# Performance work log

Measured on AMD Instinct MI355X. Metric: run time of the kernel, lower is better.

The kernel has to match this reference:

```python
import jax, jax.numpy as jnp
import numpy as np

T_MAX = 26  # hardcoded 26 char steps in the torch module

def _resize(x, hw):
    # torch F.interpolate bilinear, align_corners=False (half-pixel) == jax linear, no antialias
    return jax.image.resize(x, x.shape[:-2] + hw, method='linear', antialias=False)

def _ce(logits, labels):
    # per-element cross entropy, labels int
    logp = jax.nn.log_softmax(logits, axis=-1)
    return -jnp.take_along_axis(logp, labels[:, None].astype(jnp.int32), axis=-1)[:, 0]


def setup_inputs() -> dict:
    key = jax.random.key(0)
    ks = jax.random.split(key, 6)
    b, H, W, L = 512, 32, 128, 64
    hm, wm, hl, wl = 16, 64, 8, 32
    return {
        'masks': jax.random.uniform(ks[0], (b, 1, H, W), dtype=jnp.float32),
        'backfore_feature': jax.random.normal(ks[1], (b, 2, H, W), dtype=jnp.float32),
        'seq1_attention_map': jax.random.uniform(ks[2], (b, L, T_MAX), dtype=jnp.float32),
        'char_middle': jax.random.normal(ks[3], (b, 27, hm, wm), dtype=jnp.float32),
        'char_low': jax.random.normal(ks[4], (b, 27, hl, wl), dtype=jnp.float32),
        'length': jax.random.randint(ks[5], (b,), 2, 27),
        'iteration': 1000,
        'alpha': jnp.float32(0.1),
    }


def reference(masks, backfore_feature, seq1_attention_map, char_middle, char_low, length, iteration, alpha):
    b, _, H, W = masks.shape
    f32 = masks.dtype
    masks_i = (masks > 0.5).astype(jnp.int32)                      # [b,1,H,W]
    sm = jax.nn.softmax(backfore_feature, axis=1)                  # [b,2,H,W]

    # ---- SegLoss: CE applied to softmax probs as if logits (faithful to torch) ----
    per_elem = _ce(sm.transpose(0, 2, 3, 1).reshape(-1, 2), masks_i.reshape(-1))
    if iteration > 20000:
        value = per_elem.reshape(b, -1).mean(1)
        sel = (value < 1.0).astype(f32)
        predmask_loss = (value * sel).sum() / jnp.maximum(sel.sum(), 1.0)
    else:
        predmask_loss = per_elem.mean()

    fore_mask = (sm[:, 1] > 0.5).astype(jnp.int32)[:, None]        # [b,1,H,W], int -> no grad
    Attn = jnp.transpose(seq1_attention_map, (0, 2, 1))            # [b,26,L]
    n = length - 1                                                  # valid chars per sample
    nf = n.astype(f32)
    row_valid = (jnp.arange(T_MAX)[None, :] < n[:, None]).astype(f32)  # [b,26]

    # ---- Correct_1D_Location (seg mask detached; Attn gets grads) ----
    fore_d = jax.lax.stop_gradient(fore_mask)
    interp = _resize(Attn[:, None], (T_MAX, W))[:, 0]              # [b,26,W]
    # pairwise sum_{i<j} sum_w (v_i v_j)^2 over the first n rows, vectorized
    sq = jnp.square(interp) * row_valid[:, :, None]
    S = sq.sum(1)
    S2 = jnp.square(sq).sum(1)
    irrelevant = (0.5 * (jnp.square(S) - S2).sum(-1) / nf).sum()
    act = jax.nn.sigmoid(70.0 * (interp - 0.1)) * row_valid[:, :, None]
    # sum_t act[t,w] * mask[h,w] == (sum_t act)[w] * mask[h,w]
    char_sum = jnp.clip(act.sum(1)[:, None, :] * fore_d[:, 0].astype(f32), 0.0, 1.0)  # [b,H,W]
    single2 = jnp.stack([1.0 - char_sum, char_sum], axis=-1)       # [b,H,W,2]
    correct_loss = _ce(single2.reshape(-1, 2), fore_d.reshape(-1)).mean() + irrelevant

    # ---- Char_Segmention_Loss (attention and fore mask detached) ----
    attn_clr = jax.lax.stop_gradient(Attn) * row_valid[:, :, None]  # clear_noise

    def char_branch(char_feat):
        h, w = char_feat.shape[2], char_feat.shape[3]
        fm = (_resize(fore_d.astype(f32), (h, w)) >= 0.4).astype(jnp.int32)   # [b,1,h,w]
        ai = _resize(attn_clr[:, None], (T_MAX, w))[:, 0]
        ab = (ai > alpha).astype(jnp.int32)                                   # [b,26,w]
        single = ab[:, :, None, :] * fm                                       # [b,26,h,w]
        mask27 = jnp.concatenate([1 - fm, single], axis=1)                    # [b,27,h,w]
        labels = jnp.argmax(mask27, axis=1).reshape(-1)
        cel = _ce(char_feat.transpose(0, 2, 3, 1).reshape(-1, 27), labels).mean()
        soft = jax.nn.softmax(char_feat, axis=1)
        m1 = soft[:, 1:].reshape(b, T_MAX, -1)
        m2 = mask27[:, 1:].astype(f32).reshape(b, T_MAX, -1)
        inter = (m1 * m2).sum(-1)
        score = (2.0 * inter + 1.0) / (m1.sum(-1) + m2.sum(-1) + 1.0)         # [b,26]
        dice = (((1.0 - score) * row_valid).sum(-1) / nf).sum() / b
        return cel + dice, mask27, soft

    loss_middle, _, soft_mid = char_branch(char_middle)
    loss_low, mask_low, soft_low = char_branch(char_low)

    return (predmask_loss, correct_loss, loss_low, loss_middle,
            mask_low, soft_mid[:, 1:], soft_low[:, 1:])
```

## Files before the change

### kernel.cpp

```cpp
#include <hip/hip_runtime.h>
#include <math.h>

#define NB 512
#define TT 26
#define LL 64
#define HH 32
#define WW 128

typedef unsigned long long ull;

__device__ __forceinline__ float wave_sum(float v) {
#pragma unroll
  for (int o = 32; o > 0; o >>= 1) v += __shfl_xor(v, o, 64);
  return v;
}

template<int CTRL, int RM>
__device__ __forceinline__ float dpp_add(float x) {
  int y = __builtin_amdgcn_update_dpp(0, __float_as_int(x), CTRL, RM, 0xf, true);
  return x + __int_as_float(y);
}
__device__ __forceinline__ float wave_red63(float x) {
  x = dpp_add<0x111, 0xf>(x);
  x = dpp_add<0x112, 0xf>(x);
  x = dpp_add<0x114, 0xf>(x);
  x = dpp_add<0x118, 0xf>(x);
  x = dpp_add<0x142, 0xa>(x);
  x = dpp_add<0x143, 0xc>(x);
  return x;
}

__global__ __launch_bounds__(1024) void k_mega(
    const float* __restrict__ masks, const float* __restrict__ bf,
    const float* __restrict__ seq, const float* __restrict__ cm,
    const float* __restrict__ cl, const int* __restrict__ length,
    const float* __restrict__ alpha_p,
    float* __restrict__ out_mask, float* __restrict__ out_smid,
    float* __restrict__ out_slow,
    float* __restrict__ seg_part, float* __restrict__ cor_part,
    float* __restrict__ irr_part, float* __restrict__ celm_part,
    float* __restrict__ cell_part,
    float* __restrict__ inter_mid, float* __restrict__ m1s_mid, float* __restrict__ m2s_mid,
    float* __restrict__ inter_low, float* __restrict__ m1s_low, float* __restrict__ m2s_low)
{
  int b = blockIdx.x;
  int tid = threadIdx.x;
  int lane = tid & 63, wv = tid >> 6;

  __shared__ float att[LL * TT];
  __shared__ float wsA_lds[WW];
  __shared__ ull s_bits[TT];
  __shared__ unsigned s_alow[TT];
  __shared__ unsigned s_cols_mid[64];
  __shared__ unsigned s_cols_low[32];
  __shared__ ull fmsk_lds[64];
  __shared__ ull s_fmrow[16];
  __shared__ unsigned fmrow32[8];
  __shared__ float s_red_in[16][TT], s_red_m1[16][TT];
  __shared__ float s_ce[16];
  __shared__ float ps[16], pc[16];
  __shared__ float wpart[2];

  int n = length[b] - 1;
  float alpha = alpha_p[0];

  const float* sb = seq + (size_t)b * (LL * TT);
  for (int i = tid; i < LL * TT; i += 1024) att[i] = sb[i];
  __syncthreads();

  if (tid < 128) {
    int w = tid;
    int k = w >> 1;
    int i0, i1; float c0, c1;
    if ((w & 1) == 0) {
      if (k == 0) { i0 = 0; i1 = 0; c0 = 1.f; c1 = 0.f; }
      else        { i0 = k - 1; i1 = k; c0 = 0.25f; c1 = 0.75f; }
    } else {
      if (k == 63) { i0 = 63; i1 = 63; c0 = 1.f; c1 = 0.f; }
      else         { i0 = k; i1 = k + 1; c0 = 0.75f; c1 = 0.25f; }
    }
    float S = 0.f, S2 = 0.f, A = 0.f;
    for (int t = 0; t < n; ++t) {
      float v = c0 * att[i0 * TT + t] + c1 * att[i1 * TT + t];
      float s = v * v;
      S += s; S2 += s * s;
      A += 1.f / (1.f + __expf(-70.f * (v - 0.1f)));
    }
    wsA_lds[w] = A;
    float c = S * S - S2;
    c = wave_sum(c);
    if (lane == 0) wpart[wv] = c;
  }
  if (tid < 64) {
    int x = tid;
    for (int t = 0; t < TT; ++t) {
      bool pred = (t < n) && (att[x * TT + t] > alpha);
      ull m = __ballot(pred);
      if (x == 0) s_bits[t] = m;
    }
  } else if (tid < 128) {
    int x = tid - 64;
    for (int t = 0; t < TT; ++t) {
      bool pred = (x < 32) && (t < n) &&
                  (0.5f * (att[(2 * x) * TT + t] + att[(2 * x + 1) * TT + t]) > alpha);
      ull m = __ballot(pred);
      if (x == 0) s_alow[t] = (unsigned)m;
    }
  }
  __syncthreads();
  if (tid == 0) irr_part[b] = 0.5f * (wpart[0] + wpart[1]) / (float)n;

  if (tid < 64) {
    unsigned cb = 0;
#pragma unroll
    for (int t = 0; t < TT; ++t) cb |= (unsigned)((s_bits[t] >> tid) & 1ULL) << t;
    s_cols_mid[tid] = cb;
  } else if (tid < 96) {
    int xc = tid - 64;
    unsigned cb = 0;
#pragma unroll
    for (int t = 0; t < TT; ++t) cb |= ((s_alow[t] >> xc) & 1u) << t;
    s_cols_low[xc] = cb;
  }

  {
    const float* mb = masks + (size_t)b * 4096;
    const float* fb = bf + (size_t)b * 8192;
    float A = wsA_lds[tid & 127];
    float cs = fminf(fmaxf(A, 0.f), 1.f);
    float ce_fore = log1pf(__expf(1.f - 2.f * cs));
    float seg_acc = 0.f, cor_acc = 0.f;
    for (int k = 0; k < 4; ++k) {
      int px = k * 1024 + tid;
      float m = mb[px];
      float b0 = fb[px];
      float b1 = fb[4096 + px];
      float mx = fmaxf(b0, b1);
      float e0 = __expf(b0 - mx), e1 = __expf(b1 - mx);
      float inv = 1.f / (e0 + e1);
      float p0 = e0 * inv, p1 = e1 * inv;
      float pm = fmaxf(p0, p1);
      float lse = pm + log1pf(__expf(-fabsf(p1 - p0)));
      seg_acc += lse - ((m > 0.5f) ? p1 : p0);
      bool fore = b1 > b0;
      cor_acc += fore ? ce_fore : 0.313261687518222834f;
      ull fbm = __ballot(fore);
      if (lane == 0) fmsk_lds[k * 16 + wv] = fbm;
    }
    seg_acc = wave_red63(seg_acc);
    cor_acc = wave_red63(cor_acc);
    if (lane == 63) { ps[wv] = seg_acc; pc[wv] = cor_acc; }
  }
  __syncthreads();
  if (tid == 0) {
    float s = 0.f, c = 0.f;
#pragma unroll
    for (int i = 0; i < 16; ++i) { s += ps[i]; c += pc[i]; }
    seg_part[b] = s;
    cor_part[b] = c;
  }

  {
    int y = wv;
    int x = tid & 63;
    int word = x >> 5;
    int p = (x & 31) * 2;
    ull r0 = fmsk_lds[4 * y + word];
    ull r1 = fmsk_lds[4 * y + 2 + word];
    int cnt = (int)((r0 >> p) & 1) + (int)((r0 >> (p + 1)) & 1)
            + (int)((r1 >> p) & 1) + (int)((r1 >> (p + 1)) & 1);
    bool fm = cnt >= 2;
    unsigned cbk = s_cols_mid[x];
    int lab = (fm && cbk) ? __ffs((int)cbk) : 0;
    if (!fm) cbk = 0;
    ull bmv = __ballot(fm);
    if (lane == 0) s_fmrow[wv] = bmv;

    const float* base = cm + (size_t)b * 27 * 1024 + tid;
    float v[27];
    float xl = 0.f, s0 = 0.f;
#pragma unroll
    for (int c = 0; c < 27; ++c) {
      float r = base[(size_t)c * 1024];
      xl = (c == lab) ? r : xl;
      r = __expf(r);
      v[c] = r;
      s0 += r;
    }
    float inv0 = 1.f / s0;
    float ce_part = __logf(s0) - xl;

    float* os = out_smid + (size_t)b * 26 * 1024 + tid;
#pragma unroll
    for (int t = 0; t < TT; ++t) {
      float m1 = v[t + 1] * inv0;
      os[(size_t)t * 1024] = m1;
      float ri = wave_red63(((cbk >> t) & 1) ? m1 : 0.f);
      float rm = wave_red63(m1);
      if (lane == 63) { s_red_in[wv][t] = ri; s_red_m1[wv][t] = rm; }
    }
    float rce = wave_red63(ce_part);
    if (lane == 63) s_ce[wv] = rce;
  }
  __syncthreads();
  if (tid < TT) {
    float m2v = 0.f;
#pragma unroll
    for (int r = 0; r < 16; ++r) m2v += (float)__popcll(s_fmrow[r] & s_bits[tid]);
    float si = 0.f, sm = 0.f;
#pragma unroll
    for (int w = 0; w < 16; ++w) { si += s_red_in[w][tid]; sm += s_red_m1[w][tid]; }
    int o = b * TT + tid;
    m2s_mid[o] = m2v;
    inter_mid[o] = si;
    m1s_mid[o] = sm;
  }
  if (tid == TT) {
    float c16 = 0.f;
#pragma unroll
    for (int w = 0; w < 16; ++w) c16 += s_ce[w];
    celm_part[b] = c16;
  }
  __syncthreads();

  if (tid < 256) {
    int px = tid;
    int y = px >> 5, x = px & 31;
    int wb = 4 * x + 1;
    int word = wb >> 6;
    int p = wb & 63;
    ull r0 = fmsk_lds[(4 * y + 1) * 2 + word];
    ull r1 = fmsk_lds[(4 * y + 2) * 2 + word];
    int cnt = (int)((r0 >> p) & 1) + (int)((r0 >> (p + 1)) & 1)
            + (int)((r1 >> p) & 1) + (int)((r1 >> (p + 1)) & 1);
    bool fm = cnt >= 2;
    unsigned cbk = s_cols_low[x];
    int lab = (fm && cbk) ? __ffs((int)cbk) : 0;
    if (!fm) cbk = 0;
    ull bmv = __ballot(fm);
    if (lane == 0) {
      fmrow32[2 * wv] = (unsigned)bmv;
      fmrow32[2 * wv + 1] = (unsigned)(bmv >> 32);
    }

    const float* base = cl + (size_t)b * 27 * 256 + px;
    float v[27];
    float xl = 0.f, s0 = 0.f;
#pragma unroll
    for (int c = 0; c < 27; ++c) {
      float r = base[(size_t)c * 256];
      xl = (c == lab) ? r : xl;
      r = __expf(r);
      v[c] = r;
      s0 += r;
    }
    float inv0 = 1.f / s0;
    float ce_part = __logf(s0) - xl;

    float* om  = out_mask + (size_t)b * 27 * 256 + px;
    float* osf = out_slow + (size_t)b * 26 * 256 + px;
    om[0] = fm ? 0.f : 1.f;
#pragma unroll
    for (int t = 0; t < TT; ++t) {
      float m1 = v[t + 1] * inv0;
      osf[(size_t)t * 256] = m1;
      bool m2 = (cbk >> t) & 1;
      om[(size_t)(t + 1) * 256] = m2 ? 1.f : 0.f;
      float ri = wave_red63(m2 ? m1 : 0.f);
      float rm = wave_red63(m1);
      if (lane == 63) { s_red_in[wv][t] = ri; s_red_m1[wv][t] = rm; }
    }
    float rce = wave_red63(ce_part);
    if (lane == 63) s_ce[wv] = rce;
  }
  __syncthreads();
  if (tid < TT) {
    float m2v = 0.f;
#pragma unroll
    for (int yy = 0; yy < 8; ++yy) m2v += (float)__popc(fmrow32[yy] & s_alow[tid]);
    float si = 0.f, sm = 0.f;
#pragma unroll
    for (int w = 0; w < 4; ++w) { si += s_red_in[w][tid]; sm += s_red_m1[w][tid]; }
    int o = b * TT + tid;
    m2s_low[o] = m2v;
    inter_low[o] = si;
    m1s_low[o] = sm;
  }
  if (tid == TT) cell_part[b] = s_ce[0] + s_ce[1] + s_ce[2] + s_ce[3];
}

__global__ __launch_bounds__(1024) void k_final(
    const float* __restrict__ seg_part, const float* __restrict__ cor_part,
    const float* __restrict__ irr_part, const float* __restrict__ celm_part,
    const float* __restrict__ cell_part,
    const float* __restrict__ inter_mid, const float* __restrict__ m1s_mid,
    const float* __restrict__ m2s_mid,
    const float* __restrict__ inter_low, const float* __restrict__ m1s_low,
    const float* __restrict__ m2s_low,
    const int* __restrict__ length, const int* __restrict__ iter_p,
    float* __restrict__ out)
{
  int tid = threadIdx.x;
  float dm = 0.f, dl = 0.f;
  for (int i = tid; i < NB * TT; i += 1024) {
    int b = i / TT, t = i - b * TT;
    int n = length[b] - 1;
    if (t < n) {
      float inv_n = 1.f / (float)n;
      dm += (1.f - (2.f * inter_mid[i] + 1.f) / (m1s_mid[i] + m2s_mid[i] + 1.f)) * inv_n;
      dl += (1.f - (2.f * inter_low[i] + 1.f) / (m1s_low[i] + m2s_low[i] + 1.f)) * inv_n;
    }
  }
  float ss = 0.f, sel = 0.f, ssel = 0.f;
  float irr = 0.f, cell = 0.f, celm = 0.f, cor = 0.f;
  for (int b = tid; b < NB; b += 1024) {
    float v = seg_part[b];
    ss += v;
    float val = v * (1.f / 4096.f);
    if (val < 1.f) { sel += 1.f; ssel += val; }
    irr += irr_part[b]; cell += cell_part[b]; celm += celm_part[b]; cor += cor_part[b];
  }

  dm = wave_sum(dm); dl = wave_sum(dl); ss = wave_sum(ss);
  sel = wave_sum(sel); ssel = wave_sum(ssel);
  irr = wave_sum(irr); celm = wave_sum(celm); cell = wave_sum(cell);
  cor = wave_sum(cor);
  __shared__ float red[9][16];
  int wv = tid >> 6;
  if ((tid & 63) == 0) {
    red[0][wv] = dm; red[1][wv] = dl; red[2][wv] = ss; red[3][wv] = sel;
    red[4][wv] = ssel; red[5][wv] = irr; red[6][wv] = celm; red[7][wv] = cell;
    red[8][wv] = cor;
  }
  __syncthreads();
  if (tid == 0) {
    float a[9];
#pragma unroll
    for (int j = 0; j < 9; ++j) {
      float s = 0.f;
      for (int i = 0; i < 16; ++i) s += red[j][i];
      a[j] = s;
    }
    float pred = (iter_p[0] > 20000) ? (a[4] / fmaxf(a[3], 1.f)) : (a[2] / 2097152.f);
    out[0] = pred;
    out[1] = a[8] / 2097152.f + a[5];
    out[2] = a[7] / 131072.f + a[1] / 512.f;
    out[3] = a[6] / 524288.f + a[0] / 512.f;
  }
}

extern "C" void kernel_launch(void* const* d_in, const int* in_sizes, int n_in,
                              void* d_out, int out_size, void* d_ws, size_t ws_size,
                              hipStream_t stream) {
  (void)in_sizes; (void)n_in; (void)out_size; (void)ws_size;
  const float* masks  = (const float*)d_in[0];
  const float* bf     = (const float*)d_in[1];
  const float* seq    = (const float*)d_in[2];
  const float* cmid   = (const float*)d_in[3];
  const float* clow   = (const float*)d_in[4];
  const int*   length = (const int*)d_in[5];
  const int*   iter   = (const int*)d_in[6];
  const float* alpha  = (const float*)d_in[7];
  float* out = (float*)d_out;

  char* ws = (char*)d_ws;
  float* seg_part  = (float*)(ws + 0);
  float* cor_part  = (float*)(ws + 2048);
  float* irr_part  = (float*)(ws + 4096);
  float* celm_part = (float*)(ws + 6144);
  float* cell_part = (float*)(ws + 8192);
  float* inter_mid = (float*)(ws + 10240);
  float* m1s_mid   = (float*)(ws + 63488);
  float* m2s_mid   = (float*)(ws + 116736);
  float* inter_low = (float*)(ws + 169984);
  float* m1s_low   = (float*)(ws + 223232);
  float* m2s_low   = (float*)(ws + 276480);

  float* out_mask = out + 4;
  float* out_smid = out + 4 + 3538944;
  float* out_slow = out + 4 + 3538944 + 13631488;

  k_mega<<<NB, 1024, 0, stream>>>(masks, bf, seq, cmid, clow, length, alpha,
                                  out_mask, out_smid, out_slow,
                                  seg_part, cor_part, irr_part, celm_part, cell_part,
                                  inter_mid, m1s_mid, m2s_mid,
                                  inter_low, m1s_low, m2s_low);
  k_final<<<1, 1024, 0, stream>>>(seg_part, cor_part, irr_part, celm_part, cell_part,
                                  inter_mid, m1s_mid, m2s_mid,
                                  inter_low, m1s_low, m2s_low, length, iter, out);
}
```

Baseline: 65.63 us.

## Split mega kernel into pre-pass and LDS-staged char kernel with vectorized I/O

The single per-sample mega kernel is split into a small 256-thread pre-pass, which computes the seg/correct losses and the attention and foreground bitmasks into workspace, and a character kernel. The character kernel stages the char logits and softmax outputs through LDS so global loads and stores use float4, and it replaces per-t wave reductions with per-wave column sums. The low-resolution branch gets its own blocks, each handling four samples, so it runs in parallel with the mid branch. The cost is an extra kernel launch, a workspace round trip for the bitmasks, and about 62KB of LDS per block, which limits occupancy.

```diff
diff --git a/kernel.cpp b/kernel.cpp
--- a/kernel.cpp
+++ b/kernel.cpp
@@ -3,11 +3,9 @@
 
 #define NB 512
 #define TT 26
-#define LL 64
-#define HH 32
-#define WW 128
 
 typedef unsigned long long ull;
+typedef unsigned int u32;
 
 __device__ __forceinline__ float wave_sum(float v) {
 #pragma unroll
@@ -30,47 +28,27 @@
   return x;
 }
 
-__global__ __launch_bounds__(1024) void k_mega(
+__global__ __launch_bounds__(256) void k_pre(
     const float* __restrict__ masks, const float* __restrict__ bf,
-    const float* __restrict__ seq, const float* __restrict__ cm,
-    const float* __restrict__ cl, const int* __restrict__ length,
+    const float* __restrict__ seq, const int* __restrict__ length,
     const float* __restrict__ alpha_p,
-    float* __restrict__ out_mask, float* __restrict__ out_smid,
-    float* __restrict__ out_slow,
+    ull* __restrict__ amid, u32* __restrict__ alow, ull* __restrict__ fmsk,
     float* __restrict__ seg_part, float* __restrict__ cor_part,
-    float* __restrict__ irr_part, float* __restrict__ celm_part,
-    float* __restrict__ cell_part,
-    float* __restrict__ inter_mid, float* __restrict__ m1s_mid, float* __restrict__ m2s_mid,
-    float* __restrict__ inter_low, float* __restrict__ m1s_low, float* __restrict__ m2s_low)
+    float* __restrict__ irr_part)
 {
-  int b = blockIdx.x;
-  int tid = threadIdx.x;
-  int lane = tid & 63, wv = tid >> 6;
-
-  __shared__ float att[LL * TT];
-  __shared__ float wsA_lds[WW];
-  __shared__ ull s_bits[TT];
-  __shared__ unsigned s_alow[TT];
-  __shared__ unsigned s_cols_mid[64];
-  __shared__ unsigned s_cols_low[32];
-  __shared__ ull fmsk_lds[64];
-  __shared__ ull s_fmrow[16];
-  __shared__ unsigned fmrow32[8];
-  __shared__ float s_red_in[16][TT], s_red_m1[16][TT];
-  __shared__ float s_ce[16];
-  __shared__ float ps[16], pc[16];
-  __shared__ float wpart[2];
-
+  int b = blockIdx.x, tid = threadIdx.x, lane = tid & 63, wv = tid >> 6;
+  __shared__ float att[64 * TT];
+  __shared__ float wsA[128];
+  __shared__ float wpart[2], ps[4], pc[4];
+  const float4* sb4 = (const float4*)(seq + (size_t)b * (64 * TT));
+  float4* att4 = (float4*)att;
+  for (int i = tid; i < 416; i += 256) att4[i] = sb4[i];
+  __syncthreads();
   int n = length[b] - 1;
   float alpha = alpha_p[0];
 
-  const float* sb = seq + (size_t)b * (LL * TT);
-  for (int i = tid; i < LL * TT; i += 1024) att[i] = sb[i];
-  __syncthreads();
-
   if (tid < 128) {
-    int w = tid;
-    int k = w >> 1;
+    int w = tid, k = w >> 1;
     int i0, i1; float c0, c1;
     if ((w & 1) == 0) {
       if (k == 0) { i0 = 0; i1 = 0; c0 = 1.f; c1 = 0.f; }
@@ -86,7 +64,7 @@
       S += s; S2 += s * s;
       A += 1.f / (1.f + __expf(-70.f * (v - 0.1f)));
     }
-    wsA_lds[w] = A;
+    wsA[w] = A;
     float c = S * S - S2;
     c = wave_sum(c);
     if (lane == 0) wpart[wv] = c;
@@ -96,7 +74,7 @@
     for (int t = 0; t < TT; ++t) {
       bool pred = (t < n) && (att[x * TT + t] > alpha);
       ull m = __ballot(pred);
-      if (x == 0) s_bits[t] = m;
+      if (x == 0) amid[(size_t)b * TT + t] = m;
     }
   } else if (tid < 128) {
     int x = tid - 64;
@@ -104,189 +82,287 @@
       bool pred = (x < 32) && (t < n) &&
                   (0.5f * (att[(2 * x) * TT + t] + att[(2 * x + 1) * TT + t]) > alpha);
       ull m = __ballot(pred);
-      if (x == 0) s_alow[t] = (unsigned)m;
+      if (x == 0) alow[(size_t)b * TT + t] = (u32)m;
     }
   }
   __syncthreads();
   if (tid == 0) irr_part[b] = 0.5f * (wpart[0] + wpart[1]) / (float)n;
 
-  if (tid < 64) {
-    unsigned cb = 0;
-#pragma unroll
-    for (int t = 0; t < TT; ++t) cb |= (unsigned)((s_bits[t] >> tid) & 1ULL) << t;
-    s_cols_mid[tid] = cb;
-  } else if (tid < 96) {
-    int xc = tid - 64;
-    unsigned cb = 0;
-#pragma unroll
-    for (int t = 0; t < TT; ++t) cb |= ((s_alow[t] >> xc) & 1u) << t;
-    s_cols_low[xc] = cb;
-  }
-
-  {
-    const float* mb = masks + (size_t)b * 4096;
-    const float* fb = bf + (size_t)b * 8192;
-    float A = wsA_lds[tid & 127];
-    float cs = fminf(fmaxf(A, 0.f), 1.f);
-    float ce_fore = log1pf(__expf(1.f - 2.f * cs));
-    float seg_acc = 0.f, cor_acc = 0.f;
-    for (int k = 0; k < 4; ++k) {
-      int px = k * 1024 + tid;
-      float m = mb[px];
-      float b0 = fb[px];
-      float b1 = fb[4096 + px];
-      float mx = fmaxf(b0, b1);
-      float e0 = __expf(b0 - mx), e1 = __expf(b1 - mx);
-      float inv = 1.f / (e0 + e1);
-      float p0 = e0 * inv, p1 = e1 * inv;
-      float pm = fmaxf(p0, p1);
-      float lse = pm + log1pf(__expf(-fabsf(p1 - p0)));
-      seg_acc += lse - ((m > 0.5f) ? p1 : p0);
-      bool fore = b1 > b0;
-      cor_acc += fore ? ce_fore : 0.313261687518222834f;
-      ull fbm = __ballot(fore);
-      if (lane == 0) fmsk_lds[k * 16 + wv] = fbm;
-    }
-    seg_acc = wave_red63(seg_acc);
-    cor_acc = wave_red63(cor_acc);
-    if (lane == 63) { ps[wv] = seg_acc; pc[wv] = cor_acc; }
-  }
+  const float* mb = masks + (size_t)b * 4096;
+  const float* fb = bf + (size_t)b * 8192;
+  float A = wsA[tid & 127];
+  float cs = fminf(fmaxf(A, 0.f), 1.f);
+  float ce_fore = log1pf(__expf(1.f - 2.f * cs));
+  float seg_acc = 0.f, cor_acc = 0.f;
+  for (int k = 0; k < 16; ++k) {
+    int px = k * 256 + tid;
+    float m = mb[px];
+    float b0 = fb[px];
+    float b1 = fb[4096 + px];
+    float mx = fmaxf(b0, b1);
+    float e0 = __expf(b0 - mx), e1 = __expf(b1 - mx);
+    float inv = 1.f / (e0 + e1);
+    float p0 = e0 * inv, p1 = e1 * inv;
+    float pm = fmaxf(p0, p1);
+    float lse = pm + log1pf(__expf(-fabsf(p1 - p0)));
+    seg_acc += lse - ((m > 0.5f) ? p1 : p0);
+    bool fore = b1 > b0;
+    cor_acc += fore ? ce_fore : 0.313261687518222834f;
+    ull fbm = __ballot(fore);
+    if (lane == 0) fmsk[(size_t)b * 64 + k * 4 + wv] = fbm;
+  }
+  seg_acc = wave_red63(seg_acc);
+  cor_acc = wave_red63(cor_acc);
+  if (lane == 63) { ps[wv] = seg_acc; pc[wv] = cor_acc; }
   __syncthreads();
   if (tid == 0) {
-    float s = 0.f, c = 0.f;
-#pragma unroll
-    for (int i = 0; i < 16; ++i) { s += ps[i]; c += pc[i]; }
-    seg_part[b] = s;
-    cor_part[b] = c;
-  }
-
-  {
-    int y = wv;
-    int x = tid & 63;
-    int word = x >> 5;
-    int p = (x & 31) * 2;
-    ull r0 = fmsk_lds[4 * y + word];
-    ull r1 = fmsk_lds[4 * y + 2 + word];
+    seg_part[b] = ps[0] + ps[1] + ps[2] + ps[3];
+    cor_part[b] = pc[0] + pc[1] + pc[2] + pc[3];
+  }
+}
+
+__global__ __launch_bounds__(1024) void k_chars(
+    const float* __restrict__ cm, const float* __restrict__ cl,
+    const ull* __restrict__ fmsk, const ull* __restrict__ amid,
+    const u32* __restrict__ alow,
+    float* __restrict__ out_mask, float* __restrict__ out_smid,
+    float* __restrict__ out_slow,
+    float* __restrict__ celm_part, float* __restrict__ cell_part,
+    float* __restrict__ inter_mid, float* __restrict__ m1s_mid, float* __restrict__ m2s_mid,
+    float* __restrict__ inter_low, float* __restrict__ m1s_low, float* __restrict__ m2s_low)
+{
+  int blk = blockIdx.x, tid = threadIdx.x, lane = tid & 63, wv = tid >> 6;
+  __shared__ __align__(16) char smem[62816];
+
+  if (blk < NB) {
+    float*  bufF   = (float*)smem;
+    float4* buf4   = (float4*)smem;
+    u32*    cbkA   = (u32*)(smem + 57344);
+    ull*    s_bits = (ull*)(smem + 61440);
+    ull*    s_fmw  = (ull*)(smem + 61648);
+    u32*    s_cols = (u32*)(smem + 62160);
+    ull*    s_fmrow= (ull*)(smem + 62416);
+    float*  red_in = (float*)(smem + 62544);
+    float*  red_m1 = (float*)(smem + 62648);
+    float*  s_ce   = (float*)(smem + 62752);
+    int b = blk, px = tid, x = lane, y = wv;
+
+    if (tid < TT) s_bits[tid] = amid[(size_t)b * TT + tid];
+    else if (tid >= 32 && tid < 96) s_fmw[tid - 32] = fmsk[(size_t)b * 64 + (tid - 32)];
+    const float4* cm4 = (const float4*)(cm + (size_t)b * 27648);
+    for (int i = tid; i < 3584; i += 1024) buf4[i] = cm4[i];
+    __syncthreads();
+    if (tid < 64) {
+      u32 cb = 0;
+#pragma unroll
+      for (int t = 0; t < TT; ++t) cb |= (u32)((s_bits[t] >> tid) & 1ULL) << t;
+      s_cols[tid] = cb;
+    }
+    float v[27];
+#pragma unroll
+    for (int c = 0; c < 14; ++c) v[c] = bufF[c * 1024 + px];
+    __syncthreads();
+    for (int i = tid; i < 3328; i += 1024) buf4[i] = cm4[3584 + i];
+    __syncthreads();
+#pragma unroll
+    for (int c = 14; c < 27; ++c) v[c] = bufF[(c - 14) * 1024 + px];
+
+    int word = x >> 5, p = (x & 31) * 2;
+    ull r0 = s_fmw[4 * y + word], r1 = s_fmw[4 * y + 2 + word];
     int cnt = (int)((r0 >> p) & 1) + (int)((r0 >> (p + 1)) & 1)
             + (int)((r1 >> p) & 1) + (int)((r1 >> (p + 1)) & 1);
     bool fm = cnt >= 2;
-    unsigned cbk = s_cols_mid[x];
+    u32 cbk = s_cols[x];
     int lab = (fm && cbk) ? __ffs((int)cbk) : 0;
     if (!fm) cbk = 0;
     ull bmv = __ballot(fm);
     if (lane == 0) s_fmrow[wv] = bmv;
-
-    const float* base = cm + (size_t)b * 27 * 1024 + tid;
-    float v[27];
+    cbkA[px] = cbk;
+
     float xl = 0.f, s0 = 0.f;
 #pragma unroll
     for (int c = 0; c < 27; ++c) {
-      float r = base[(size_t)c * 1024];
+      float r = v[c];
       xl = (c == lab) ? r : xl;
-      r = __expf(r);
-      v[c] = r;
-      s0 += r;
+      float e = __expf(r);
+      v[c] = e;
+      s0 += e;
     }
     float inv0 = 1.f / s0;
-    float ce_part = __logf(s0) - xl;
-
-    float* os = out_smid + (size_t)b * 26 * 1024 + tid;
-#pragma unroll
-    for (int t = 0; t < TT; ++t) {
-      float m1 = v[t + 1] * inv0;
-      os[(size_t)t * 1024] = m1;
-      float ri = wave_red63(((cbk >> t) & 1) ? m1 : 0.f);
-      float rm = wave_red63(m1);
-      if (lane == 63) { s_red_in[wv][t] = ri; s_red_m1[wv][t] = rm; }
-    }
-    float rce = wave_red63(ce_part);
+    float rce = wave_red63(__logf(s0) - xl);
     if (lane == 63) s_ce[wv] = rce;
-  }
-  __syncthreads();
-  if (tid < TT) {
-    float m2v = 0.f;
-#pragma unroll
-    for (int r = 0; r < 16; ++r) m2v += (float)__popcll(s_fmrow[r] & s_bits[tid]);
-    float si = 0.f, sm = 0.f;
-#pragma unroll
-    for (int w = 0; w < 16; ++w) { si += s_red_in[w][tid]; sm += s_red_m1[w][tid]; }
-    int o = b * TT + tid;
-    m2s_mid[o] = m2v;
-    inter_mid[o] = si;
-    m1s_mid[o] = sm;
-  }
-  if (tid == TT) {
-    float c16 = 0.f;
-#pragma unroll
-    for (int w = 0; w < 16; ++w) c16 += s_ce[w];
-    celm_part[b] = c16;
-  }
-  __syncthreads();
-
-  if (tid < 256) {
-    int px = tid;
-    int y = px >> 5, x = px & 31;
-    int wb = 4 * x + 1;
-    int word = wb >> 6;
-    int p = wb & 63;
-    ull r0 = fmsk_lds[(4 * y + 1) * 2 + word];
-    ull r1 = fmsk_lds[(4 * y + 2) * 2 + word];
-    int cnt = (int)((r0 >> p) & 1) + (int)((r0 >> (p + 1)) & 1)
-            + (int)((r1 >> p) & 1) + (int)((r1 >> (p + 1)) & 1);
-    bool fm = cnt >= 2;
-    unsigned cbk = s_cols_low[x];
-    int lab = (fm && cbk) ? __ffs((int)cbk) : 0;
-    if (!fm) cbk = 0;
-    ull bmv = __ballot(fm);
-    if (lane == 0) {
-      fmrow32[2 * wv] = (unsigned)bmv;
-      fmrow32[2 * wv + 1] = (unsigned)(bmv >> 32);
-    }
-
-    const float* base = cl + (size_t)b * 27 * 256 + px;
-    float v[27];
-    float xl = 0.f, s0 = 0.f;
-#pragma unroll
-    for (int c = 0; c < 27; ++c) {
-      float r = base[(size_t)c * 256];
-      xl = (c == lab) ? r : xl;
-      r = __expf(r);
-      v[c] = r;
-      s0 += r;
-    }
-    float inv0 = 1.f / s0;
-    float ce_part = __logf(s0) - xl;
-
-    float* om  = out_mask + (size_t)b * 27 * 256 + px;
-    float* osf = out_slow + (size_t)b * 26 * 256 + px;
-    om[0] = fm ? 0.f : 1.f;
-#pragma unroll
-    for (int t = 0; t < TT; ++t) {
-      float m1 = v[t + 1] * inv0;
-      osf[(size_t)t * 256] = m1;
-      bool m2 = (cbk >> t) & 1;
-      om[(size_t)(t + 1) * 256] = m2 ? 1.f : 0.f;
-      float ri = wave_red63(m2 ? m1 : 0.f);
-      float rm = wave_red63(m1);
-      if (lane == 63) { s_red_in[wv][t] = ri; s_red_m1[wv][t] = rm; }
-    }
-    float rce = wave_red63(ce_part);
-    if (lane == 63) s_ce[wv] = rce;
-  }
-  __syncthreads();
-  if (tid < TT) {
-    float m2v = 0.f;
-#pragma unroll
-    for (int yy = 0; yy < 8; ++yy) m2v += (float)__popc(fmrow32[yy] & s_alow[tid]);
-    float si = 0.f, sm = 0.f;
-#pragma unroll
-    for (int w = 0; w < 4; ++w) { si += s_red_in[w][tid]; sm += s_red_m1[w][tid]; }
-    int o = b * TT + tid;
-    m2s_low[o] = m2v;
-    inter_low[o] = si;
-    m1s_low[o] = sm;
-  }
-  if (tid == TT) cell_part[b] = s_ce[0] + s_ce[1] + s_ce[2] + s_ce[3];
+
+#pragma unroll
+    for (int t = 13; t < 26; ++t) bufF[(t - 13) * 1024 + px] = v[t + 1] * inv0;
+    __syncthreads();
+    float4* smid4 = (float4*)(out_smid + (size_t)b * 26624);
+    for (int i = tid; i < 3328; i += 1024) smid4[3328 + i] = buf4[i];
+    if (wv < 13) {
+      int t = 13 + wv;
+      float isum = 0.f, msum = 0.f;
+#pragma unroll
+      for (int k = 0; k < 16; ++k) {
+        int q = lane + 64 * k;
+        float m1 = bufF[wv * 1024 + q];
+        u32 cb = cbkA[q];
+        msum += m1;
+        isum += ((cb >> t) & 1) ? m1 : 0.f;
+      }
+      isum = wave_red63(isum); msum = wave_red63(msum);
+      if (lane == 63) { red_in[t] = isum; red_m1[t] = msum; }
+    }
+    __syncthreads();
+#pragma unroll
+    for (int t = 0; t < 13; ++t) bufF[t * 1024 + px] = v[t + 1] * inv0;
+    __syncthreads();
+    for (int i = tid; i < 3328; i += 1024) smid4[i] = buf4[i];
+    if (wv < 13) {
+      int t = wv;
+      float isum = 0.f, msum = 0.f;
+#pragma unroll
+      for (int k = 0; k < 16; ++k) {
+        int q = lane + 64 * k;
+        float m1 = bufF[wv * 1024 + q];
+        u32 cb = cbkA[q];
+        msum += m1;
+        isum += ((cb >> t) & 1) ? m1 : 0.f;
+      }
+      isum = wave_red63(isum); msum = wave_red63(msum);
+      if (lane == 63) { red_in[t] = isum; red_m1[t] = msum; }
+    }
+    __syncthreads();
+    if (tid < TT) {
+      float m2v = 0.f;
+#pragma unroll
+      for (int r = 0; r < 16; ++r) m2v += (float)__popcll(s_fmrow[r] & s_bits[tid]);
+      int o = b * TT + tid;
+      m2s_mid[o] = m2v;
+      inter_mid[o] = red_in[tid];
+      m1s_mid[o] = red_m1[tid];
+    }
+    if (tid == TT) {
+      float c16 = 0.f;
+#pragma unroll
+      for (int w = 0; w < 16; ++w) c16 += s_ce[w];
+      celm_part[b] = c16;
+    }
+  } else {
+    int L = blk - NB;
+    float*  bufF    = (float*)smem;
+    float4* buf4    = (float4*)smem;
+    u32*    cbkL    = (u32*)(smem + 55296);
+    u32*    l_bits  = (u32*)(smem + 57344);
+    u32*    colsL   = (u32*)(smem + 57760);
+    ull*    fmw4    = (ull*)(smem + 58272);
+    u32*    fmrow32 = (u32*)(smem + 60320);
+    float*  ceL     = (float*)(smem + 60384);
+
+    if (tid < 104) l_bits[tid] = alow[(size_t)(L * 4) * TT + tid];
+    else if (tid >= 128 && tid < 384) fmw4[tid - 128] = fmsk[(size_t)(L * 4) * 64 + (tid - 128)];
+    __syncthreads();
+    if (tid < 128) {
+      int s = tid >> 5, xx = tid & 31;
+      u32 cb = 0;
+#pragma unroll
+      for (int t = 0; t < TT; ++t) cb |= ((l_bits[s * TT + t] >> xx) & 1u) << t;
+      colsL[tid] = cb;
+    }
+    const float4* cl4 = (const float4*)cl;
+    float4* slow4 = (float4*)out_slow;
+    float4* mask4 = (float4*)out_mask;
+
+    for (int pr = 0; pr < 2; ++pr) {
+      for (int i = tid; i < 3456; i += 1024) {
+        int s = i / 1728, r = i - s * 1728;
+        buf4[i] = cl4[(size_t)(L * 4 + 2 * pr + s) * 1728 + r];
+      }
+      __syncthreads();
+      if (tid < 512) {
+        int s = tid >> 8, sl = 2 * pr + s;
+        int px = tid & 255, y = px >> 5, xx = px & 31;
+        int wb = 4 * xx + 1, word = wb >> 6, pp = wb & 63;
+        ull r0 = fmw4[sl * 64 + (4 * y + 1) * 2 + word];
+        ull r1 = fmw4[sl * 64 + (4 * y + 2) * 2 + word];
+        int cnt = (int)((r0 >> pp) & 1) + (int)((r0 >> (pp + 1)) & 1)
+                + (int)((r1 >> pp) & 1) + (int)((r1 >> (pp + 1)) & 1);
+        bool fm = cnt >= 2;
+        u32 cbk = colsL[sl * 32 + xx];
+        int lab = (fm && cbk) ? __ffs((int)cbk) : 0;
+        if (!fm) cbk = 0;
+        ull bmv = __ballot(fm);
+        if (lane == 0) {
+          fmrow32[s * 8 + 2 * (wv & 3)] = (u32)bmv;
+          fmrow32[s * 8 + 2 * (wv & 3) + 1] = (u32)(bmv >> 32);
+        }
+        float v[27];
+#pragma unroll
+        for (int c = 0; c < 27; ++c) v[c] = bufF[s * 6912 + c * 256 + px];
+        float xl = 0.f, s0 = 0.f;
+#pragma unroll
+        for (int c = 0; c < 27; ++c) {
+          float r = v[c];
+          xl = (c == lab) ? r : xl;
+          float e = __expf(r);
+          v[c] = e;
+          s0 += e;
+        }
+        float inv0 = 1.f / s0;
+        float rce = wave_red63(__logf(s0) - xl);
+        if (lane == 63) ceL[wv] = rce;
+        bufF[s * 6912 + px] = fm ? 0.f : 1.f;
+#pragma unroll
+        for (int t = 0; t < TT; ++t) bufF[s * 6912 + (t + 1) * 256 + px] = v[t + 1] * inv0;
+        cbkL[s * 256 + px] = cbk;
+      }
+      __syncthreads();
+      for (int i = tid; i < 3328; i += 1024) {
+        int s = i / 1664, r = i - s * 1664;
+        slow4[(size_t)(L * 4 + 2 * pr + s) * 1664 + r] = buf4[s * 1728 + 64 + r];
+      }
+      for (int i = tid; i < 3456; i += 1024) {
+        int s = i / 1728, r = i - s * 1728;
+        int c = r >> 6, off = r & 63;
+        float4 o;
+        if (c == 0) o = buf4[s * 1728 + off];
+        else {
+          int t = c - 1;
+          o.x = ((cbkL[s * 256 + off * 4 + 0] >> t) & 1) ? 1.f : 0.f;
+          o.y = ((cbkL[s * 256 + off * 4 + 1] >> t) & 1) ? 1.f : 0.f;
+          o.z = ((cbkL[s * 256 + off * 4 + 2] >> t) & 1) ? 1.f : 0.f;
+          o.w = ((cbkL[s * 256 + off * 4 + 3] >> t) & 1) ? 1.f : 0.f;
+        }
+        mask4[(size_t)(L * 4 + 2 * pr + s) * 1728 + r] = o;
+      }
+      if (tid < 512) {
+        int s = wv >> 2;
+        int bb2 = L * 4 + 2 * pr + s;
+        for (int t = wv & 3; t < TT; t += 4) {
+          float isum = 0.f, msum = 0.f;
+#pragma unroll
+          for (int k = 0; k < 4; ++k) {
+            int q = lane + 64 * k;
+            float m1 = bufF[s * 6912 + (t + 1) * 256 + q];
+            u32 cb = cbkL[s * 256 + q];
+            msum += m1;
+            isum += ((cb >> t) & 1) ? m1 : 0.f;
+          }
+          isum = wave_red63(isum); msum = wave_red63(msum);
+          if (lane == 63) { inter_low[bb2 * TT + t] = isum; m1s_low[bb2 * TT + t] = msum; }
+        }
+      }
+      if (tid >= 512 && tid < 564) {
+        int j = tid - 512;
+        int s = j / TT, t = j - s * TT, sl = 2 * pr + s;
+        float m2v = 0.f;
+#pragma unroll
+        for (int yy = 0; yy < 8; ++yy) m2v += (float)__popc(fmrow32[s * 8 + yy] & l_bits[sl * TT + t]);
+        m2s_low[(L * 4 + sl) * TT + t] = m2v;
+      }
+      if (tid == 600) cell_part[L * 4 + 2 * pr] = ceL[0] + ceL[1] + ceL[2] + ceL[3];
+      if (tid == 601) cell_part[L * 4 + 2 * pr + 1] = ceL[4] + ceL[5] + ceL[6] + ceL[7];
+      __syncthreads();
+    }
+  }
 }
 
 __global__ __launch_bounds__(1024) void k_final(
@@ -320,7 +396,6 @@
     if (val < 1.f) { sel += 1.f; ssel += val; }
     irr += irr_part[b]; cell += cell_part[b]; celm += celm_part[b]; cor += cor_part[b];
   }
-
   dm = wave_sum(dm); dl = wave_sum(dl); ss = wave_sum(ss);
   sel = wave_sum(sel); ssel = wave_sum(ssel);
   irr = wave_sum(irr); celm = wave_sum(celm); cell = wave_sum(cell);
@@ -375,16 +450,21 @@
   float* inter_low = (float*)(ws + 169984);
   float* m1s_low   = (float*)(ws + 223232);
   float* m2s_low   = (float*)(ws + 276480);
+  ull* amid = (ull*)(ws + 329728);
+  u32* alow = (u32*)(ws + 436224);
+  ull* fmsk = (ull*)(ws + 489472);
 
   float* out_mask = out + 4;
   float* out_smid = out + 4 + 3538944;
   float* out_slow = out + 4 + 3538944 + 13631488;
 
-  k_mega<<<NB, 1024, 0, stream>>>(masks, bf, seq, cmid, clow, length, alpha,
-                                  out_mask, out_smid, out_slow,
-                                  seg_part, cor_part, irr_part, celm_part, cell_part,
-                                  inter_mid, m1s_mid, m2s_mid,
-                                  inter_low, m1s_low, m2s_low);
+  k_pre<<<NB, 256, 0, stream>>>(masks, bf, seq, length, alpha,
+                                amid, alow, fmsk, seg_part, cor_part, irr_part);
+  k_chars<<<NB + NB / 4, 1024, 0, stream>>>(cmid, clow, fmsk, amid, alow,
+                                            out_mask, out_smid, out_slow,
+                                            celm_part, cell_part,
+                                            inter_mid, m1s_mid, m2s_mid,
+                                            inter_low, m1s_low, m2s_low);
   k_final<<<1, 1024, 0, stream>>>(seg_part, cor_part, irr_part, celm_part, cell_part,
                                   inter_mid, m1s_mid, m2s_mid,
                                   inter_low, m1s_low, m2s_low, length, iter, out);
```

New measurement: 67.39 us. 1.03x slower.
